# Kernel tuning notes

Hardware: AMD Instinct MI355X
Metric: run time of the kernel (lower is better)

Reference implementation:

```python
import jax, jax.numpy as jnp
import numpy as np

IN_DIM = 128
NUM_IDX = 128
LATENT = 512
FF_HID = 4 * IN_DIM
EPS = 1e-5


def _layernorm(x, g, b):
    mu = jnp.mean(x, axis=-1, keepdims=True)
    var = jnp.mean((x - mu) ** 2, axis=-1, keepdims=True)
    return (x - mu) * jax.lax.rsqrt(var + EPS) * g + b


def setup_inputs() -> dict:
    key = jax.random.key(0)
    ks = jax.random.split(key, 12)
    B, N, D, L = 16, NUM_IDX, IN_DIM, LATENT
    s = lambda fan_in: 1.0 / np.sqrt(fan_in)
    return {
        "in_obs": jax.random.normal(ks[0], (B, N, D), jnp.float32),
        "Wq_w": jax.random.normal(ks[1], (D, L), jnp.float32) * s(D),
        "Wq_b": jax.random.normal(ks[2], (L,), jnp.float32) * s(D),
        "Wk_w": jax.random.normal(ks[3], (D, L), jnp.float32) * s(D),
        "Wk_b": jax.random.normal(ks[4], (L,), jnp.float32) * s(D),
        "wv_w": jax.random.normal(ks[5], (2 * L + 2 * N,), jnp.float32) * s(2 * L + 2 * N),
        "wv_b": jax.random.normal(ks[6], (), jnp.float32) * s(2 * L + 2 * N),
        "g1": jnp.ones((D,), jnp.float32),
        "b1": jnp.zeros((D,), jnp.float32),
        "ff1_w": jax.random.normal(ks[7], (D, FF_HID), jnp.float32) * s(D),
        "ff1_b": jax.random.normal(ks[8], (FF_HID,), jnp.float32) * s(D),
        "ff2_w": jax.random.normal(ks[9], (FF_HID, D), jnp.float32) * s(FF_HID),
        "ff2_b": jax.random.normal(ks[10], (D,), jnp.float32) * s(FF_HID),
        "g2": jnp.ones((D,), jnp.float32),
        "b2": jnp.zeros((D,), jnp.float32),
    }


def reference(in_obs, Wq_w, Wq_b, Wk_w, Wk_b, wv_w, wv_b, g1, b1,
              ff1_w, ff1_b, ff2_w, ff2_b, g2, b2):
    # in_obs: [B, N, D]
    B, N, D = in_obs.shape
    L = Wq_w.shape[1]
    eye = jnp.broadcast_to(jnp.eye(N, dtype=in_obs.dtype), (B, N, N))
    # q_cat/k_cat: [B, N, L+N]
    q_cat = jnp.concatenate([in_obs @ Wq_w + Wq_b, eye], axis=-1)
    k_cat = jnp.concatenate([in_obs @ Wk_w + Wk_b, eye], axis=-1)
    # Original: w_v(tanh(concat(q_i, k_j))). tanh is elementwise and the dot
    # product splits over the concat, so score[b,i,j] = a[b,i] + c[b,j] + bias
    # -- mathematically identical, avoids the [B,N,N,2L+2N] intermediate.
    a = jnp.tanh(q_cat) @ wv_w[: L + N]          # [B, N]
    c = jnp.tanh(k_cat) @ wv_w[L + N:]           # [B, N]
    scores = a[:, :, None] + c[:, None, :] + wv_b  # [B, N, N]
    weights = jax.nn.softmax(scores, axis=-1)
    attn = weights @ in_obs                       # [B, N, D]
    res = _layernorm(attn + in_obs, g1, b1)
    ff = jax.nn.relu(res @ ff1_w + ff1_b) @ ff2_w + ff2_b
    return _layernorm(ff + in_obs, g2, b2)
```

## Files before the change

kernel.cpp:

```cpp
#include <hip/hip_runtime.h>

#define NN 128
#define DD 128
#define LL 512
#define FFH 512
#define TANH1 0.76159415595576489f

typedef __attribute__((ext_vector_type(8))) short bf16x8;
typedef __attribute__((ext_vector_type(4))) float f32x4;

struct alignas(16) f4arr { float v[4]; };

__device__ __forceinline__ unsigned short f2bf(float f) {
    union { float f; unsigned u; } v; v.f = f;
    return (unsigned short)((v.u + 0x7FFFu + ((v.u >> 16) & 1u)) >> 16);
}

__global__ __launch_bounds__(256) void kA(
    const float* __restrict__ in_obs,
    const float* __restrict__ Wk_w,
    const float* __restrict__ Wk_b,
    const float* __restrict__ wv_w,
    const float* __restrict__ ff1_w,
    const float* __restrict__ ff2_w,
    float* __restrict__ c_out,
    unsigned short* __restrict__ W1f,
    unsigned short* __restrict__ W2f)
{
    const int t = threadIdx.x;
    const int wave = t >> 6, lane = t & 63;
    __shared__ float row_lds[8][128];
    __shared__ float red[8][4];

    if (blockIdx.x >= 256) {
        const int bi = blockIdx.x - 256;
        const int l15 = lane & 15, l4 = lane >> 4;
        const int fg = (bi & 31) * 4 + wave;
        unsigned short vals[8];
        unsigned short* dst;
        if (bi < 32) {
            const int ks = fg & 3, mt = fg >> 2;
            #pragma unroll
            for (int j = 0; j < 8; ++j)
                vals[j] = f2bf(ff1_w[(ks * 32 + l4 * 8 + j) * FFH + mt * 16 + l15]);
            dst = W1f;
        } else {
            const int ks = fg & 15, mt = fg >> 4;
            #pragma unroll
            for (int j = 0; j < 8; ++j)
                vals[j] = f2bf(ff2_w[(ks * 32 + l4 * 8 + j) * DD + mt * 16 + l15]);
            dst = W2f;
        }
        uint4 u;
        u.x = (unsigned)vals[0] | ((unsigned)vals[1] << 16);
        u.y = (unsigned)vals[2] | ((unsigned)vals[3] << 16);
        u.z = (unsigned)vals[4] | ((unsigned)vals[5] << 16);
        u.w = (unsigned)vals[6] | ((unsigned)vals[7] << 16);
        *(uint4*)&dst[(fg * 64 + lane) * 8] = u;
        return;
    }

    const int row0 = blockIdx.x * 8;
    const float* src = in_obs + row0 * DD;
    #pragma unroll
    for (int i = 0; i < 4; ++i) {
        int idx = t + i * 256;
        row_lds[idx >> 7][idx & 127] = src[idx];
    }
    __syncthreads();

    const int l0 = t, l1 = t + 256;
    float acc0[8], acc1[8];
    #pragma unroll
    for (int r = 0; r < 8; ++r) { acc0[r] = 0.f; acc1[r] = 0.f; }

    #pragma unroll 4
    for (int d = 0; d < 128; d += 4) {
        f4arr rbuf[8];
        #pragma unroll
        for (int r = 0; r < 8; ++r)
            rbuf[r] = *(const f4arr*)&row_lds[r][d];
        #pragma unroll
        for (int dd = 0; dd < 4; ++dd) {
            const float w0 = Wk_w[(d + dd) * LL + l0];
            const float w1 = Wk_w[(d + dd) * LL + l1];
            #pragma unroll
            for (int r = 0; r < 8; ++r) {
                acc0[r] += rbuf[r].v[dd] * w0;
                acc1[r] += rbuf[r].v[dd] * w1;
            }
        }
    }
    const float kb0 = Wk_b[l0], kb1 = Wk_b[l1];
    const float wv0 = wv_w[640 + l0], wv1 = wv_w[640 + l1];
    float v[8];
    #pragma unroll
    for (int r = 0; r < 8; ++r)
        v[r] = tanhf(acc0[r] + kb0) * wv0 + tanhf(acc1[r] + kb1) * wv1;
    #pragma unroll
    for (int off = 32; off > 0; off >>= 1) {
        #pragma unroll
        for (int r = 0; r < 8; ++r)
            v[r] += __shfl_down(v[r], off, 64);
    }
    if (lane == 0) {
        #pragma unroll
        for (int r = 0; r < 8; ++r) red[r][wave] = v[r];
    }
    __syncthreads();
    if (t < 8) {
        const int row = row0 + t;
        const int j = row & (NN - 1);
        c_out[row] = red[t][0] + red[t][1] + red[t][2] + red[t][3]
                   + TANH1 * wv_w[1152 + j];
    }
}

__global__ __launch_bounds__(1024) void kB(
    const float* __restrict__ in_obs,
    const float* __restrict__ c_in,
    const unsigned short* __restrict__ W1f,
    const unsigned short* __restrict__ W2f,
    const float* __restrict__ g1, const float* __restrict__ b1,
    const float* __restrict__ ff1_b,
    const float* __restrict__ ff2_b,
    const float* __restrict__ g2, const float* __restrict__ b2,
    float* __restrict__ out)
{
    const int t = threadIdx.x;
    const int b = blockIdx.x >> 4;
    const int j0 = (blockIdx.x & 15) * 8;
    const int wave = t >> 6, lane = t & 63;
    const int l15 = lane & 15, l4 = lane >> 4;

    __shared__ alignas(16) unsigned short res_lds[16 * 128];
    __shared__ alignas(16) unsigned short h_lds[16 * 512];
    __shared__ alignas(16) float o2p[2][2048];
    __shared__ float part[8][128];

    bf16x8 a1[2][4];
    #pragma unroll
    for (int i = 0; i < 2; ++i)
        #pragma unroll
        for (int ks = 0; ks < 4; ++ks)
            a1[i][ks] = *(const bf16x8*)(W1f + (((wave * 2 + i) * 4 + ks) * 64 + lane) * 8);
    bf16x8 a2[8];
    {
        const int n = wave & 7, kh = wave >> 3;
        #pragma unroll
        for (int k2 = 0; k2 < 8; ++k2)
            a2[k2] = *(const bf16x8*)(W2f + ((n * 16 + kh * 8 + k2) * 64 + lane) * 8);
    }

    const int r = wave & 7;
    const int row = b * NN + j0 + r;
    const int c0i = lane * 2;
    float2 xo, g1v, b1v, g2v, b2v, f2bv;
    if (wave < 8) {
        xo   = *(const float2*)&in_obs[row * DD + c0i];
        g1v  = *(const float2*)&g1[c0i];  b1v = *(const float2*)&b1[c0i];
        g2v  = *(const float2*)&g2[c0i];  b2v = *(const float2*)&b2[c0i];
        f2bv = *(const float2*)&ff2_b[c0i];
    }

    const float* cb = c_in + b * NN;
    float c0 = cb[lane], c1 = cb[lane + 64];
    float mx = fmaxf(c0, c1);
    #pragma unroll
    for (int off = 32; off > 0; off >>= 1) mx = fmaxf(mx, __shfl_xor(mx, off, 64));
    float e0 = __expf(c0 - mx), e1 = __expf(c1 - mx);
    float sm = e0 + e1;
    #pragma unroll
    for (int off = 32; off > 0; off >>= 1) sm += __shfl_xor(sm, off, 64);
    const float inv = 1.f / sm;
    e0 *= inv; e1 *= inv;

    {
        const int grp = wave >> 1, d = (wave & 1) * 64 + lane;
        const float* base = in_obs + (b * NN + grp * 16) * DD + d;
        float acc = 0.f;
        #pragma unroll
        for (int jj = 0; jj < 16; ++jj) {
            const int j = grp * 16 + jj;
            const float wj = (grp < 4) ? __shfl(e0, j & 63, 64)
                                       : __shfl(e1, j & 63, 64);
            acc += wj * base[jj * DD];
        }
        part[grp][d] = acc;
    }
    __syncthreads();

    if (wave < 8) {
        float x0 = xo.x, x1 = xo.y;
        #pragma unroll
        for (int g = 0; g < 8; ++g) { x0 += part[g][c0i]; x1 += part[g][c0i + 1]; }
        float s = x0 + x1;
        #pragma unroll
        for (int off = 32; off > 0; off >>= 1) s += __shfl_xor(s, off, 64);
        const float mu = s * (1.f / 128.f);
        const float d0 = x0 - mu, d1 = x1 - mu;
        float vs = d0 * d0 + d1 * d1;
        #pragma unroll
        for (int off = 32; off > 0; off >>= 1) vs += __shfl_xor(vs, off, 64);
        const float rstd = rsqrtf(vs * (1.f / 128.f) + 1e-5f);
        const float r0 = d0 * rstd * g1v.x + b1v.x;
        const float r1 = d1 * rstd * g1v.y + b1v.y;
        const unsigned pk = (unsigned)f2bf(r0) | ((unsigned)f2bf(r1) << 16);
        const int swz = (lane * 4) ^ ((r & 7) << 4);
        *(unsigned*)((char*)res_lds + r * 256 + swz) = pk;
        *(unsigned*)((char*)res_lds + (r + 8) * 256 + swz) = 0u;
    }
    __syncthreads();

    {
        bf16x8 bfrag[4];
        #pragma unroll
        for (int ks = 0; ks < 4; ++ks) {
            const int off = l15 * 256 + ((ks * 64 + l4 * 16) ^ ((l15 & 7) << 4));
            bfrag[ks] = *(const bf16x8*)((const char*)res_lds + off);
        }
        #pragma unroll
        for (int i = 0; i < 2; ++i) {
            const int mt = wave * 2 + i;
            f32x4 acc = {0.f, 0.f, 0.f, 0.f};
            #pragma unroll
            for (int ks = 0; ks < 4; ++ks)
                acc = __builtin_amdgcn_mfma_f32_16x16x32_bf16(a1[i][ks], bfrag[ks], acc, 0, 0, 0);
            const f4arr bias = *(const f4arr*)&ff1_b[mt * 16 + l4 * 4];
            uint2 pk;
            pk.x = (unsigned)f2bf(fmaxf(acc[0] + bias.v[0], 0.f))
                 | ((unsigned)f2bf(fmaxf(acc[1] + bias.v[1], 0.f)) << 16);
            pk.y = (unsigned)f2bf(fmaxf(acc[2] + bias.v[2], 0.f))
                 | ((unsigned)f2bf(fmaxf(acc[3] + bias.v[3], 0.f)) << 16);
            const int off = l15 * 1024 + ((mt * 32 + l4 * 8) ^ ((l15 & 7) << 4));
            *(uint2*)((char*)h_lds + off) = pk;
        }
    }
    __syncthreads();

    {
        const int n = wave & 7, kh = wave >> 3;
        f32x4 acc = {0.f, 0.f, 0.f, 0.f};
        #pragma unroll
        for (int k2 = 0; k2 < 8; ++k2) {
            const int ks = kh * 8 + k2;
            const int off = l15 * 1024 + ((ks * 64 + l4 * 16) ^ ((l15 & 7) << 4));
            const bf16x8 bfrag = *(const bf16x8*)((const char*)h_lds + off);
            acc = __builtin_amdgcn_mfma_f32_16x16x32_bf16(a2[k2], bfrag, acc, 0, 0, 0);
        }
        const int off = l15 * 512 + ((n * 64 + l4 * 16) ^ ((l15 & 7) << 4));
        *(f32x4*)((char*)o2p[kh] + off) = acc;
    }
    __syncthreads();

    if (wave < 8) {
        const int off = r * 512 + ((lane * 8) ^ ((r & 7) << 4));
        const float2 p0 = *(const float2*)((char*)o2p[0] + off);
        const float2 p1 = *(const float2*)((char*)o2p[1] + off);
        const float f0 = p0.x + p1.x + f2bv.x + xo.x;
        const float f1 = p0.y + p1.y + f2bv.y + xo.y;
        float s = f0 + f1;
        #pragma unroll
        for (int off2 = 32; off2 > 0; off2 >>= 1) s += __shfl_xor(s, off2, 64);
        const float mu = s * (1.f / 128.f);
        const float d0 = f0 - mu, d1 = f1 - mu;
        float vs = d0 * d0 + d1 * d1;
        #pragma unroll
        for (int off2 = 32; off2 > 0; off2 >>= 1) vs += __shfl_xor(vs, off2, 64);
        const float rstd = rsqrtf(vs * (1.f / 128.f) + 1e-5f);
        float2 o;
        o.x = d0 * rstd * g2v.x + b2v.x;
        o.y = d1 * rstd * g2v.y + b2v.y;
        *(float2*)&out[row * DD + c0i] = o;
    }
}

extern "C" void kernel_launch(void* const* d_in, const int* in_sizes, int n_in,
                              void* d_out, int out_size, void* d_ws, size_t ws_size,
                              hipStream_t stream) {
    const float* in_obs = (const float*)d_in[0];
    const float* Wk_w  = (const float*)d_in[3];
    const float* Wk_b  = (const float*)d_in[4];
    const float* wv_w  = (const float*)d_in[5];
    const float* g1    = (const float*)d_in[7];
    const float* b1    = (const float*)d_in[8];
    const float* ff1_w = (const float*)d_in[9];
    const float* ff1_b = (const float*)d_in[10];
    const float* ff2_w = (const float*)d_in[11];
    const float* ff2_b = (const float*)d_in[12];
    const float* g2    = (const float*)d_in[13];
    const float* b2    = (const float*)d_in[14];
    float* outp = (float*)d_out;

    unsigned short* W1f = (unsigned short*)d_ws;
    unsigned short* W2f = W1f + 65536;
    float* c_ws = (float*)((char*)d_ws + 262144);

    kA<<<320, 256, 0, stream>>>(in_obs, Wk_w, Wk_b, wv_w, ff1_w, ff2_w,
                                c_ws, W1f, W2f);
    kB<<<256, 1024, 0, stream>>>(in_obs, c_ws, W1f, W2f, g1, b1,
                                 ff1_b, ff2_b, g2, b2, outp);
}
```

Measured before the change: 26.98 us.

## Split kB into 512 blocks of 512 threads handling 4 rows each

kB now runs 512 blocks of 8 waves, each block handling 4 output rows instead of 8. The FF2 split-K across two wave halves is dropped: each wave does the full K=512 for one N tile, reading W2 fragments straight from global memory, and half of the W1 fragments are also loaded on the fly. Per-row parameter loads move later to cut register pressure. The aim is more blocks and higher occupancy (launch bounds 512,4). The cost is that weight traffic per output row doubles, and the MFMA tiles are now only a quarter filled (4 of 16 rows) instead of half.

```diff
diff --git a/kernel.cpp b/kernel.cpp
--- a/kernel.cpp
+++ b/kernel.cpp
@@ -116,7 +116,7 @@
     }
 }
 
-__global__ __launch_bounds__(1024) void kB(
+__global__ __launch_bounds__(512, 4) void kB(
     const float* __restrict__ in_obs,
     const float* __restrict__ c_in,
     const unsigned short* __restrict__ W1f,
@@ -128,47 +128,29 @@
     float* __restrict__ out)
 {
     const int t = threadIdx.x;
-    const int b = blockIdx.x >> 4;
-    const int j0 = (blockIdx.x & 15) * 8;
+    const int b = blockIdx.x >> 5;
+    const int j0 = (blockIdx.x & 31) * 4;
     const int wave = t >> 6, lane = t & 63;
     const int l15 = lane & 15, l4 = lane >> 4;
 
+    __shared__ float part[8][128];
     __shared__ alignas(16) unsigned short res_lds[16 * 128];
     __shared__ alignas(16) unsigned short h_lds[16 * 512];
-    __shared__ alignas(16) float o2p[2][2048];
-    __shared__ float part[8][128];
-
-    bf16x8 a1[2][4];
+    __shared__ alignas(16) float o2_lds[16 * 128];
+
+    bf16x8 a1p[2][4];
     #pragma unroll
     for (int i = 0; i < 2; ++i)
         #pragma unroll
         for (int ks = 0; ks < 4; ++ks)
-            a1[i][ks] = *(const bf16x8*)(W1f + (((wave * 2 + i) * 4 + ks) * 64 + lane) * 8);
-    bf16x8 a2[8];
-    {
-        const int n = wave & 7, kh = wave >> 3;
-        #pragma unroll
-        for (int k2 = 0; k2 < 8; ++k2)
-            a2[k2] = *(const bf16x8*)(W2f + ((n * 16 + kh * 8 + k2) * 64 + lane) * 8);
-    }
-
-    const int r = wave & 7;
-    const int row = b * NN + j0 + r;
-    const int c0i = lane * 2;
-    float2 xo, g1v, b1v, g2v, b2v, f2bv;
-    if (wave < 8) {
-        xo   = *(const float2*)&in_obs[row * DD + c0i];
-        g1v  = *(const float2*)&g1[c0i];  b1v = *(const float2*)&b1[c0i];
-        g2v  = *(const float2*)&g2[c0i];  b2v = *(const float2*)&b2[c0i];
-        f2bv = *(const float2*)&ff2_b[c0i];
-    }
-
-    const float* cb = c_in + b * NN;
-    float c0 = cb[lane], c1 = cb[lane + 64];
-    float mx = fmaxf(c0, c1);
+            a1p[i][ks] = *(const bf16x8*)(W1f + (((wave * 4 + i) * 4 + ks) * 64 + lane) * 8);
+
+    const float cv0 = c_in[b * NN + lane];
+    const float cv1 = c_in[b * NN + lane + 64];
+    float mx = fmaxf(cv0, cv1);
     #pragma unroll
     for (int off = 32; off > 0; off >>= 1) mx = fmaxf(mx, __shfl_xor(mx, off, 64));
-    float e0 = __expf(c0 - mx), e1 = __expf(c1 - mx);
+    float e0 = __expf(cv0 - mx), e1 = __expf(cv1 - mx);
     float sm = e0 + e1;
     #pragma unroll
     for (int off = 32; off > 0; off >>= 1) sm += __shfl_xor(sm, off, 64);
@@ -176,24 +158,32 @@
     e0 *= inv; e1 *= inv;
 
     {
-        const int grp = wave >> 1, d = (wave & 1) * 64 + lane;
-        const float* base = in_obs + (b * NN + grp * 16) * DD + d;
-        float acc = 0.f;
+        const float* base = in_obs + (b * NN + wave * 16) * DD;
+        float a0 = 0.f, a1 = 0.f;
         #pragma unroll
         for (int jj = 0; jj < 16; ++jj) {
-            const int j = grp * 16 + jj;
-            const float wj = (grp < 4) ? __shfl(e0, j & 63, 64)
-                                       : __shfl(e1, j & 63, 64);
-            acc += wj * base[jj * DD];
-        }
-        part[grp][d] = acc;
-    }
-    __syncthreads();
-
-    if (wave < 8) {
+            const int js = wave * 16 + jj;
+            const float wj = (wave < 4) ? __shfl(e0, js, 64)
+                                        : __shfl(e1, js - 64, 64);
+            a0 += wj * base[jj * DD + lane];
+            a1 += wj * base[jj * DD + 64 + lane];
+        }
+        part[wave][lane] = a0;
+        part[wave][lane + 64] = a1;
+    }
+    __syncthreads();
+
+    if (wave < 4) {
+        const int r = wave;
+        const int row = b * NN + j0 + r;
+        const int c0i = lane * 2;
+        const float2 xo = *(const float2*)&in_obs[row * DD + c0i];
         float x0 = xo.x, x1 = xo.y;
         #pragma unroll
-        for (int g = 0; g < 8; ++g) { x0 += part[g][c0i]; x1 += part[g][c0i + 1]; }
+        for (int g = 0; g < 8; ++g) {
+            const float2 p = *(const float2*)&part[g][c0i];
+            x0 += p.x; x1 += p.y;
+        }
         float s = x0 + x1;
         #pragma unroll
         for (int off = 32; off > 0; off >>= 1) s += __shfl_xor(s, off, 64);
@@ -203,12 +193,19 @@
         #pragma unroll
         for (int off = 32; off > 0; off >>= 1) vs += __shfl_xor(vs, off, 64);
         const float rstd = rsqrtf(vs * (1.f / 128.f) + 1e-5f);
-        const float r0 = d0 * rstd * g1v.x + b1v.x;
-        const float r1 = d1 * rstd * g1v.y + b1v.y;
+        const float2 gv = *(const float2*)&g1[c0i];
+        const float2 bv = *(const float2*)&b1[c0i];
+        const float r0 = d0 * rstd * gv.x + bv.x;
+        const float r1 = d1 * rstd * gv.y + bv.y;
         const unsigned pk = (unsigned)f2bf(r0) | ((unsigned)f2bf(r1) << 16);
         const int swz = (lane * 4) ^ ((r & 7) << 4);
         *(unsigned*)((char*)res_lds + r * 256 + swz) = pk;
-        *(unsigned*)((char*)res_lds + (r + 8) * 256 + swz) = 0u;
+    } else {
+        #pragma unroll
+        for (int k = 0; k < 3; ++k) {
+            const int r = wave + k * 4;
+            *(unsigned*)((char*)res_lds + r * 256 + lane * 4) = 0u;
+        }
     }
     __syncthreads();
 
@@ -220,12 +217,15 @@
             bfrag[ks] = *(const bf16x8*)((const char*)res_lds + off);
         }
         #pragma unroll
-        for (int i = 0; i < 2; ++i) {
-            const int mt = wave * 2 + i;
+        for (int i = 0; i < 4; ++i) {
+            const int mt = wave * 4 + i;
             f32x4 acc = {0.f, 0.f, 0.f, 0.f};
             #pragma unroll
-            for (int ks = 0; ks < 4; ++ks)
-                acc = __builtin_amdgcn_mfma_f32_16x16x32_bf16(a1[i][ks], bfrag[ks], acc, 0, 0, 0);
+            for (int ks = 0; ks < 4; ++ks) {
+                const bf16x8 afrag = (i < 2) ? a1p[i][ks]
+                    : *(const bf16x8*)(W1f + ((mt * 4 + ks) * 64 + lane) * 8);
+                acc = __builtin_amdgcn_mfma_f32_16x16x32_bf16(afrag, bfrag[ks], acc, 0, 0, 0);
+            }
             const f4arr bias = *(const f4arr*)&ff1_b[mt * 16 + l4 * 4];
             uint2 pk;
             pk.x = (unsigned)f2bf(fmaxf(acc[0] + bias.v[0], 0.f))
@@ -239,26 +239,29 @@
     __syncthreads();
 
     {
-        const int n = wave & 7, kh = wave >> 3;
         f32x4 acc = {0.f, 0.f, 0.f, 0.f};
         #pragma unroll
-        for (int k2 = 0; k2 < 8; ++k2) {
-            const int ks = kh * 8 + k2;
+        for (int ks = 0; ks < 16; ++ks) {
             const int off = l15 * 1024 + ((ks * 64 + l4 * 16) ^ ((l15 & 7) << 4));
             const bf16x8 bfrag = *(const bf16x8*)((const char*)h_lds + off);
-            acc = __builtin_amdgcn_mfma_f32_16x16x32_bf16(a2[k2], bfrag, acc, 0, 0, 0);
-        }
-        const int off = l15 * 512 + ((n * 64 + l4 * 16) ^ ((l15 & 7) << 4));
-        *(f32x4*)((char*)o2p[kh] + off) = acc;
-    }
-    __syncthreads();
-
-    if (wave < 8) {
+            const bf16x8 afrag = *(const bf16x8*)(W2f + ((wave * 16 + ks) * 64 + lane) * 8);
+            acc = __builtin_amdgcn_mfma_f32_16x16x32_bf16(afrag, bfrag, acc, 0, 0, 0);
+        }
+        const int off = l15 * 512 + ((wave * 64 + l4 * 16) ^ ((l15 & 7) << 4));
+        *(f32x4*)((char*)o2_lds + off) = acc;
+    }
+    __syncthreads();
+
+    if (wave < 4) {
+        const int r = wave;
+        const int row = b * NN + j0 + r;
+        const int c0i = lane * 2;
         const int off = r * 512 + ((lane * 8) ^ ((r & 7) << 4));
-        const float2 p0 = *(const float2*)((char*)o2p[0] + off);
-        const float2 p1 = *(const float2*)((char*)o2p[1] + off);
-        const float f0 = p0.x + p1.x + f2bv.x + xo.x;
-        const float f1 = p0.y + p1.y + f2bv.y + xo.y;
+        const float2 o2 = *(const float2*)((char*)o2_lds + off);
+        const float2 fb = *(const float2*)&ff2_b[c0i];
+        const float2 xo = *(const float2*)&in_obs[row * DD + c0i];
+        const float f0 = o2.x + fb.x + xo.x;
+        const float f1 = o2.y + fb.y + xo.y;
         float s = f0 + f1;
         #pragma unroll
         for (int off2 = 32; off2 > 0; off2 >>= 1) s += __shfl_xor(s, off2, 64);
@@ -268,9 +271,11 @@
         #pragma unroll
         for (int off2 = 32; off2 > 0; off2 >>= 1) vs += __shfl_xor(vs, off2, 64);
         const float rstd = rsqrtf(vs * (1.f / 128.f) + 1e-5f);
+        const float2 gv = *(const float2*)&g2[c0i];
+        const float2 bv = *(const float2*)&b2[c0i];
         float2 o;
-        o.x = d0 * rstd * g2v.x + b2v.x;
-        o.y = d1 * rstd * g2v.y + b2v.y;
+        o.x = d0 * rstd * gv.x + bv.x;
+        o.y = d1 * rstd * gv.y + bv.y;
         *(float2*)&out[row * DD + c0i] = o;
     }
 }
@@ -298,6 +303,6 @@
 
     kA<<<320, 256, 0, stream>>>(in_obs, Wk_w, Wk_b, wv_w, ff1_w, ff2_w,
                                 c_ws, W1f, W2f);
-    kB<<<256, 1024, 0, stream>>>(in_obs, c_ws, W1f, W2f, g1, b1,
-                                 ff1_b, ff2_b, g2, b2, outp);
+    kB<<<512, 512, 0, stream>>>(in_obs, c_ws, W1f, W2f, g1, b1,
+                                ff1_b, ff2_b, g2, b2, outp);
 }
```

Measured after the change: 27.76 us. 2.9% more time.
